# Kernel tuning notes

Hardware: AMD Instinct MI355X
Metric: run time of the kernel (lower is better)

## Reference

```python
import jax, jax.numpy as jnp
import numpy as np

N = 100000   # nodes
E = 1600000  # edges (avg degree 16)
D = 64       # input_dim
H = 64       # hidden_dim
C = 40       # num_classes
K = 2        # x_steps (KProp)


def setup_inputs() -> dict:
    key = jax.random.key(0)
    ks = jax.random.split(key, 8)
    x = jax.random.normal(ks[0], (N, D), dtype=jnp.float32)
    edge_src = jax.random.randint(ks[1], (E,), 0, N, dtype=jnp.int32)
    edge_dst = jax.random.randint(ks[2], (E,), 0, N, dtype=jnp.int32)
    def lin(k, fi, fo):
        b = 1.0 / np.sqrt(fi)
        return jax.random.uniform(k, (fi, fo), jnp.float32, -b, b)
    Wl1 = lin(ks[3], D, H)  # SAGEConv1 neighbor weight
    Wr1 = lin(ks[4], D, H)  # SAGEConv1 root weight
    b1 = jnp.zeros((H,), jnp.float32)
    Wl2 = lin(ks[5], H, C)
    Wr2 = lin(ks[6], H, C)
    b2 = jnp.zeros((C,), jnp.float32)
    return {"x": x, "Wl1": Wl1, "Wr1": Wr1, "b1": b1,
            "Wl2": Wl2, "Wr2": Wr2, "b2": b2,
            "edge_src": edge_src, "edge_dst": edge_dst}


def reference(x, Wl1, Wr1, b1, Wl2, Wr2, b2, edge_src, edge_dst):
    ones = jnp.ones((edge_src.shape[0],), x.dtype)
    deg = jax.ops.segment_sum(ones, edge_dst, num_segments=N)  # in-degree (adj_t row sums)
    # gcn_norm without self loops: w_e = deg[dst]^-1/2 * deg[src]^-1/2 (inf -> 0)
    dis = jnp.where(deg > 0, jax.lax.rsqrt(jnp.maximum(deg, 1.0)), 0.0)
    w = dis[edge_dst] * dis[edge_src]
    # KProp: K steps of normalized sparse matmul, 'add' aggregation
    h = x
    for _ in range(K):
        h = jax.ops.segment_sum(h[edge_src] * w[:, None], edge_dst, num_segments=N)
    cnt = jnp.maximum(deg, 1.0)[:, None]  # mean-aggr denominator (0-row safe)
    # SAGEConv1: lin_l(mean_neighbors) + lin_r(root), then selu (dropout p=0)
    agg1 = jax.ops.segment_sum(h[edge_src], edge_dst, num_segments=N) / cnt
    h1 = jax.nn.selu(agg1 @ Wl1 + h @ Wr1 + b1)
    # SAGEConv2
    agg2 = jax.ops.segment_sum(h1[edge_src], edge_dst, num_segments=N) / cnt
    out = agg2 @ Wl2 + h1 @ Wr2 + b2
    return jax.nn.softmax(out, axis=1)
```

## Files before the change

### kernel.cpp

```cpp
#include <hip/hip_runtime.h>
#include <hip/hip_bf16.h>
#include <math.h>


#define RFL(x) __builtin_amdgcn_readfirstlane(x)
#define BK_SHIFT 10
#define MAXBUCK 256

__device__ __forceinline__ float bf2f(unsigned short u) {
    return __uint_as_float((unsigned)u << 16);
}
__device__ __forceinline__ unsigned short f2bf(float f) {
    __hip_bfloat16 b = __float2bfloat16(f);
    return *reinterpret_cast<unsigned short*>(&b);
}


__global__ void init_bcursor_kernel(int* __restrict__ bcursor, int nbuck, int cap) {
    int i = blockIdx.x * blockDim.x + threadIdx.x;
    if (i < nbuck) bcursor[i] = i * cap;
}

__global__ __launch_bounds__(256) void partition_kernel(const int* __restrict__ src,
                                                        const int* __restrict__ dst,
                                                        int* __restrict__ bcursor,
                                                        unsigned int* __restrict__ temp,
                                                        int e, int nbuck, int cap) {
    __shared__ int bc[MAXBUCK];
    int t = threadIdx.x;
    int chunk = (e + gridDim.x - 1) / gridDim.x;
    int base = blockIdx.x * chunk;
    int cnt = e - base;
    if (cnt > chunk) cnt = chunk;
    if (cnt < 0) cnt = 0;
    for (int j = t; j < nbuck; j += 256) bc[j] = 0;
    __syncthreads();
    for (int i = t; i < cnt; i += 256) {
        int d = dst[base + i];
        atomicAdd(&bc[d >> BK_SHIFT], 1);
    }
    __syncthreads();
    for (int j = t; j < nbuck; j += 256) {
        int c = bc[j];
        bc[j] = (c > 0) ? atomicAdd(&bcursor[j], c) : 0;
    }
    __syncthreads();
    for (int i = t; i < cnt; i += 256) {
        int s = src[base + i];
        int d = dst[base + i];
        int bk = d >> BK_SHIFT;
        int p = atomicAdd(&bc[bk], 1);
        if (p < (bk + 1) * cap) temp[p] = ((unsigned int)s << BK_SHIFT) | (unsigned int)(d & 1023);
    }
}

__global__ __launch_bounds__(256) void bucket_csr_kernel(const unsigned int* __restrict__ temp,
                                                         const int* __restrict__ bcursor,
                                                         int* __restrict__ row_ptr,
                                                         float* __restrict__ dis,
                                                         float* __restrict__ cnt_inv,
                                                         int* __restrict__ csr_src,
                                                         int n, int cap, int nbuck, int e) {
    __shared__ int cnt3[1024];
    __shared__ int part[256];
    int b = blockIdx.x;
    int t = threadIdx.x;
    int nbeg = b << BK_SHIFT;
    int cj = 0;
    if (t < nbuck) {
        cj = bcursor[t] - t * cap;
        if (cj > cap) cj = cap;
    }
    part[t] = cj;
    __syncthreads();
    for (int off = 1; off < 256; off <<= 1) {
        int u = (t >= off) ? part[t - off] : 0;
        __syncthreads();
        part[t] += u;
        __syncthreads();
    }
    int cntb = bcursor[b] - b * cap;
    if (cntb > cap) cntb = cap;
    int bbase = part[b] - cntb;
    __syncthreads();
    for (int i = t; i < 1024; i += 256) cnt3[i] = 0;
    __syncthreads();
    const unsigned int* tb = temp + (size_t)b * cap;
    for (int i = t; i < cntb; i += 256) {
        atomicAdd(&cnt3[tb[i] & 1023u], 1);
    }
    __syncthreads();
    int d0 = cnt3[t * 4 + 0], d1 = cnt3[t * 4 + 1], d2 = cnt3[t * 4 + 2], d3 = cnt3[t * 4 + 3];
    int run = d0 + d1 + d2 + d3;
    int dd[4] = {d0, d1, d2, d3};
#pragma unroll
    for (int k = 0; k < 4; ++k) {
        int node = nbeg + t * 4 + k;
        if (node < n) {
            float fd = (float)dd[k];
            dis[node] = (dd[k] > 0) ? rsqrtf(fd) : 0.0f;
            cnt_inv[node] = 1.0f / fmaxf(fd, 1.0f);
        }
    }
    __syncthreads();
    part[t] = run;
    __syncthreads();
    for (int off = 1; off < 256; off <<= 1) {
        int u = (t >= off) ? part[t - off] : 0;
        __syncthreads();
        part[t] += u;
        __syncthreads();
    }
    int ex = part[t] - run;
    int oo[4];
    oo[0] = ex; oo[1] = ex + d0; oo[2] = ex + d0 + d1; oo[3] = ex + d0 + d1 + d2;
#pragma unroll
    for (int k = 0; k < 4; ++k) {
        cnt3[t * 4 + k] = oo[k];
        int node = nbeg + t * 4 + k;
        if (node < n) row_ptr[node] = bbase + oo[k];
    }
    if (b == nbuck - 1 && t == 0) row_ptr[n] = e;
    __syncthreads();
    for (int i = t; i < cntb; i += 256) {
        unsigned int ed = tb[i];
        int pos = atomicAdd(&cnt3[ed & 1023u], 1);
        csr_src[bbase + pos] = (int)(ed >> BK_SHIFT);
    }
}

__global__ void f2bf_kernel(const float4* __restrict__ in, ushort4* __restrict__ out, int n4) {
    int i = blockIdx.x * blockDim.x + threadIdx.x;
    if (i < n4) {
        float4 v = in[i];
        ushort4 u;
        u.x = f2bf(v.x); u.y = f2bf(v.y); u.z = f2bf(v.z); u.w = f2bf(v.w);
        out[i] = u;
    }
}

template <int TAG>
__global__ __launch_bounds__(256) void prop4bf_kernel(const ushort4* __restrict__ in4u,
                                                      ushort4* __restrict__ out4u,
                                                      const int* __restrict__ row_ptr,
                                                      const int* __restrict__ csr_src,
                                                      const float* __restrict__ dis,
                                                      int n) {
    int lane = threadIdx.x & 63;
    int g = lane >> 4;
    int l = lane & 15;
    int node = RFL(blockIdx.x * 4 + (threadIdx.x >> 6));
    if (node >= n) return;
    int beg = row_ptr[node];
    int end = row_ptr[node + 1];
    float4 acc = make_float4(0.f, 0.f, 0.f, 0.f);
    int j = beg;
    for (; j + 16 <= end; j += 16) {
        int s[4];
        ushort4 u[4];
        float w[4];
#pragma unroll
        for (int q = 0; q < 4; ++q) s[q] = csr_src[j + q * 4 + g];
#pragma unroll
        for (int q = 0; q < 4; ++q) u[q] = in4u[(size_t)s[q] * 16 + l];
#pragma unroll
        for (int q = 0; q < 4; ++q) w[q] = dis[s[q]];
#pragma unroll
        for (int q = 0; q < 4; ++q) {
            acc.x += w[q] * bf2f(u[q].x);
            acc.y += w[q] * bf2f(u[q].y);
            acc.z += w[q] * bf2f(u[q].z);
            acc.w += w[q] * bf2f(u[q].w);
        }
    }
    for (; j + 8 <= end; j += 8) {
        int s[2];
        ushort4 u[2];
        float w[2];
#pragma unroll
        for (int q = 0; q < 2; ++q) s[q] = csr_src[j + q * 4 + g];
#pragma unroll
        for (int q = 0; q < 2; ++q) u[q] = in4u[(size_t)s[q] * 16 + l];
#pragma unroll
        for (int q = 0; q < 2; ++q) w[q] = dis[s[q]];
#pragma unroll
        for (int q = 0; q < 2; ++q) {
            acc.x += w[q] * bf2f(u[q].x);
            acc.y += w[q] * bf2f(u[q].y);
            acc.z += w[q] * bf2f(u[q].z);
            acc.w += w[q] * bf2f(u[q].w);
        }
    }
    for (; j < end; j += 4) {
        int idx = j + g;
        bool valid = idx < end;
        int s = csr_src[valid ? idx : (end - 1)];
        float w = valid ? dis[s] : 0.0f;
        ushort4 u = in4u[(size_t)s * 16 + l];
        acc.x += w * bf2f(u.x);
        acc.y += w * bf2f(u.y);
        acc.z += w * bf2f(u.z);
        acc.w += w * bf2f(u.w);
    }
    acc.x += __shfl_xor(acc.x, 16); acc.x += __shfl_xor(acc.x, 32);
    acc.y += __shfl_xor(acc.y, 16); acc.y += __shfl_xor(acc.y, 32);
    acc.z += __shfl_xor(acc.z, 16); acc.z += __shfl_xor(acc.z, 32);
    acc.w += __shfl_xor(acc.w, 16); acc.w += __shfl_xor(acc.w, 32);
    if (g == 0) {
        float sc = dis[node];
        ushort4 o;
        o.x = f2bf(acc.x * sc);
        o.y = f2bf(acc.y * sc);
        o.z = f2bf(acc.z * sc);
        o.w = f2bf(acc.w * sc);
        out4u[(size_t)node * 16 + l] = o;
    }
}

__global__ __launch_bounds__(256) void prop_mean_bf_kernel(const ushort4* __restrict__ in4u,
                                                           ushort4* __restrict__ out4u,
                                                           const int* __restrict__ row_ptr,
                                                           const int* __restrict__ csr_src,
                                                           const float* __restrict__ cnt_inv,
                                                           const float4* __restrict__ r4,
                                                           const float4* __restrict__ b4,
                                                           int n) {
    int lane = threadIdx.x & 63;
    int g = lane >> 4;
    int l = lane & 15;
    int node = RFL(blockIdx.x * 4 + (threadIdx.x >> 6));
    if (node >= n) return;
    int beg = row_ptr[node];
    int end = row_ptr[node + 1];
    float4 acc = make_float4(0.f, 0.f, 0.f, 0.f);
    int j = beg;
    for (; j + 16 <= end; j += 16) {
        int s[4];
        ushort4 u[4];
#pragma unroll
        for (int q = 0; q < 4; ++q) s[q] = csr_src[j + q * 4 + g];
#pragma unroll
        for (int q = 0; q < 4; ++q) u[q] = in4u[(size_t)s[q] * 16 + l];
#pragma unroll
        for (int q = 0; q < 4; ++q) {
            acc.x += bf2f(u[q].x);
            acc.y += bf2f(u[q].y);
            acc.z += bf2f(u[q].z);
            acc.w += bf2f(u[q].w);
        }
    }
    for (; j + 8 <= end; j += 8) {
        int s[2];
        ushort4 u[2];
#pragma unroll
        for (int q = 0; q < 2; ++q) s[q] = csr_src[j + q * 4 + g];
#pragma unroll
        for (int q = 0; q < 2; ++q) u[q] = in4u[(size_t)s[q] * 16 + l];
#pragma unroll
        for (int q = 0; q < 2; ++q) {
            acc.x += bf2f(u[q].x);
            acc.y += bf2f(u[q].y);
            acc.z += bf2f(u[q].z);
            acc.w += bf2f(u[q].w);
        }
    }
    for (; j < end; j += 4) {
        int idx = j + g;
        bool valid = idx < end;
        int s = csr_src[valid ? idx : (end - 1)];
        float w = valid ? 1.0f : 0.0f;
        ushort4 u = in4u[(size_t)s * 16 + l];
        acc.x += w * bf2f(u.x);
        acc.y += w * bf2f(u.y);
        acc.z += w * bf2f(u.z);
        acc.w += w * bf2f(u.w);
    }
    acc.x += __shfl_xor(acc.x, 16); acc.x += __shfl_xor(acc.x, 32);
    acc.y += __shfl_xor(acc.y, 16); acc.y += __shfl_xor(acc.y, 32);
    acc.z += __shfl_xor(acc.z, 16); acc.z += __shfl_xor(acc.z, 32);
    acc.w += __shfl_xor(acc.w, 16); acc.w += __shfl_xor(acc.w, 32);
    if (g == 0) {
        float sc = cnt_inv[node];
        float4 ra = r4[(size_t)node * 16 + l];
        float4 bb = b4[l];
        const float scale = 1.0507009873554805f;
        const float alpha = 1.6732632423543772f;
        float t0 = acc.x * sc + ra.x + bb.x;
        float t1 = acc.y * sc + ra.y + bb.y;
        float t2 = acc.z * sc + ra.z + bb.z;
        float t3 = acc.w * sc + ra.w + bb.w;
        t0 = scale * (t0 > 0.0f ? t0 : alpha * expm1f(t0));
        t1 = scale * (t1 > 0.0f ? t1 : alpha * expm1f(t1));
        t2 = scale * (t2 > 0.0f ? t2 : alpha * expm1f(t2));
        t3 = scale * (t3 > 0.0f ? t3 : alpha * expm1f(t3));
        ushort4 o;
        o.x = f2bf(t0); o.y = f2bf(t1); o.z = f2bf(t2); o.w = f2bf(t3);
        out4u[(size_t)node * 16 + l] = o;
    }
}

__global__ __launch_bounds__(256) void prop_softmax_bf_kernel(const ushort4* __restrict__ in4u,
                                                              float* __restrict__ out,
                                                              const int* __restrict__ row_ptr,
                                                              const int* __restrict__ csr_src,
                                                              const float* __restrict__ cnt_inv,
                                                              const float* __restrict__ r_add,
                                                              int n) {
    int lane = threadIdx.x & 63;
    int g = lane >> 4;
    int l = lane & 15;
    bool act = l < 10;
    int node = RFL(blockIdx.x * 4 + (threadIdx.x >> 6));
    if (node >= n) return;
    int beg = row_ptr[node];
    int end = row_ptr[node + 1];
    float4 acc = make_float4(0.f, 0.f, 0.f, 0.f);
    const ushort4 uz = make_ushort4(0, 0, 0, 0);
    int j = beg;
    for (; j + 16 <= end; j += 16) {
        int s[4];
        ushort4 u[4] = {uz, uz, uz, uz};
#pragma unroll
        for (int q = 0; q < 4; ++q) s[q] = csr_src[j + q * 4 + g];
        if (act) {
#pragma unroll
            for (int q = 0; q < 4; ++q) u[q] = in4u[(size_t)s[q] * 10 + l];
        }
#pragma unroll
        for (int q = 0; q < 4; ++q) {
            acc.x += bf2f(u[q].x);
            acc.y += bf2f(u[q].y);
            acc.z += bf2f(u[q].z);
            acc.w += bf2f(u[q].w);
        }
    }
    for (; j + 8 <= end; j += 8) {
        int s[2];
        ushort4 u[2] = {uz, uz};
#pragma unroll
        for (int q = 0; q < 2; ++q) s[q] = csr_src[j + q * 4 + g];
        if (act) {
#pragma unroll
            for (int q = 0; q < 2; ++q) u[q] = in4u[(size_t)s[q] * 10 + l];
        }
#pragma unroll
        for (int q = 0; q < 2; ++q) {
            acc.x += bf2f(u[q].x);
            acc.y += bf2f(u[q].y);
            acc.z += bf2f(u[q].z);
            acc.w += bf2f(u[q].w);
        }
    }
    for (; j < end; j += 4) {
        int idx = j + g;
        bool valid = idx < end;
        int s = csr_src[valid ? idx : (end - 1)];
        if (act) {
            ushort4 u = in4u[(size_t)s * 10 + l];
            float w = valid ? 1.0f : 0.0f;
            acc.x += w * bf2f(u.x);
            acc.y += w * bf2f(u.y);
            acc.z += w * bf2f(u.z);
            acc.w += w * bf2f(u.w);
        }
    }
    acc.x += __shfl_xor(acc.x, 16); acc.x += __shfl_xor(acc.x, 32);
    acc.y += __shfl_xor(acc.y, 16); acc.y += __shfl_xor(acc.y, 32);
    acc.z += __shfl_xor(acc.z, 16); acc.z += __shfl_xor(acc.z, 32);
    acc.w += __shfl_xor(acc.w, 16); acc.w += __shfl_xor(acc.w, 32);
    if (g == 0) {
        float sc = cnt_inv[node];
        float4 ra = act ? reinterpret_cast<const float4*>(r_add)[(size_t)node * 10 + l]
                        : make_float4(0.f, 0.f, 0.f, 0.f);
        float t0 = acc.x * sc + ra.x;
        float t1 = acc.y * sc + ra.y;
        float t2 = acc.z * sc + ra.z;
        float t3 = acc.w * sc + ra.w;
        float m = act ? fmaxf(fmaxf(t0, t1), fmaxf(t2, t3)) : -INFINITY;
        m = fmaxf(m, __shfl_xor(m, 1));
        m = fmaxf(m, __shfl_xor(m, 2));
        m = fmaxf(m, __shfl_xor(m, 4));
        m = fmaxf(m, __shfl_xor(m, 8));
        float e0 = act ? __expf(t0 - m) : 0.0f;
        float e1 = act ? __expf(t1 - m) : 0.0f;
        float e2 = act ? __expf(t2 - m) : 0.0f;
        float e3 = act ? __expf(t3 - m) : 0.0f;
        float s = e0 + e1 + e2 + e3;
        s += __shfl_xor(s, 1);
        s += __shfl_xor(s, 2);
        s += __shfl_xor(s, 4);
        s += __shfl_xor(s, 8);
        if (act) {
            float inv = 1.0f / s;
            float4 o;
            o.x = e0 * inv; o.y = e1 * inv; o.z = e2 * inv; o.w = e3 * inv;
            reinterpret_cast<float4*>(out)[(size_t)node * 10 + l] = o;
        }
    }
}

template <int OC, int CP>
__global__ __launch_bounds__(256) void gemm_kernel(const unsigned short* __restrict__ in,
                                                   const float* __restrict__ Wl,
                                                   const float* __restrict__ Wr,
                                                   const float* __restrict__ bias,
                                                   __hip_bfloat16* __restrict__ outL,
                                                   float* __restrict__ outR,
                                                   int n, int add_bias) {
    constexpr int HC = OC / 2;
    constexpr int TX = OC / CP;
    constexpr int TY = 256 / TX;
    constexpr int NPT = 64 / TY;
    constexpr int XP = 68;
    constexpr int WP = OC + 4;
    __shared__ float sXT[64 * XP];
    __shared__ float sW[64 * WP];
    int t = threadIdx.x;
    int blk = blockIdx.x;
    for (int i = 0; i < 16; ++i) {
        int idx = i * 256 + t;
        int nd = idx >> 6;
        int k = idx & 63;
        int ng = blk * 64 + nd;
        float v = bf2f(in[(size_t)(ng < n ? ng : n - 1) * 64 + k]);
        sXT[k * XP + nd] = v;
    }
    for (int i = t; i < 64 * HC; i += 256) {
        int k = i / HC;
        int c = i % HC;
        sW[k * WP + c] = Wl[i];
        sW[k * WP + HC + c] = Wr[i];
    }
    __syncthreads();
    int tx = t % TX;
    int ty = t / TX;
    float acc[NPT][CP];
#pragma unroll
    for (int i = 0; i < NPT; ++i)
#pragma unroll
        for (int c = 0; c < CP; ++c) acc[i][c] = 0.0f;
#pragma unroll 4
    for (int k = 0; k < 64; ++k) {
        float xv[NPT];
#pragma unroll
        for (int i = 0; i < NPT; ++i) xv[i] = sXT[k * XP + ty * NPT + i];
        float wv[CP];
#pragma unroll
        for (int c = 0; c < CP; ++c) wv[c] = sW[k * WP + tx + TX * c];
#pragma unroll
        for (int i = 0; i < NPT; ++i)
#pragma unroll
            for (int c = 0; c < CP; ++c) acc[i][c] += xv[i] * wv[c];
    }
#pragma unroll
    for (int i = 0; i < NPT; ++i) {
        int ng = blk * 64 + ty * NPT + i;
        if (ng >= n) break;
#pragma unroll
        for (int c = 0; c < CP; ++c) {
            int col = tx + TX * c;
            if (col < HC) {
                outL[(size_t)ng * HC + col] = __float2bfloat16(acc[i][c]);
            } else {
                float v = acc[i][c] + (add_bias ? bias[col - HC] : 0.0f);
                outR[(size_t)ng * HC + (col - HC)] = v;
            }
        }
    }
}


extern "C" void kernel_launch(void* const* d_in, const int* in_sizes, int n_in,
                              void* d_out, int out_size, void* d_ws, size_t ws_size,
                              hipStream_t stream) {
    const float* x   = (const float*)d_in[0];
    const float* Wl1 = (const float*)d_in[1];
    const float* Wr1 = (const float*)d_in[2];
    const float* b1  = (const float*)d_in[3];
    const float* Wl2 = (const float*)d_in[4];
    const float* Wr2 = (const float*)d_in[5];
    const float* b2  = (const float*)d_in[6];
    const int* edge_src = (const int*)d_in[7];
    const int* edge_dst = (const int*)d_in[8];
    float* out = (float*)d_out;

    const int N = in_sizes[0] / 64;
    const int E = in_sizes[7];
    const int NBUCK = (N + (1 << BK_SHIFT) - 1) >> BK_SHIFT;
    size_t buf_bytes = (size_t)N * 64 * 4;
    int cap = E / NBUCK + E / (2 * NBUCK) + 1024;
    int cap_max = (int)(buf_bytes / ((size_t)NBUCK * 4));
    if (cap > cap_max) cap = cap_max;

    size_t off = 0;
    auto carve = [&](size_t bytes) -> void* {
        void* p = (char*)d_ws + off;
        off = (off + bytes + 255) & ~(size_t)255;
        return p;
    };
    int*          row_ptr = (int*)carve((size_t)(N + 1) * 4);
    int*          bcursor = (int*)carve((size_t)NBUCK * 4);
    float*        dis     = (float*)carve((size_t)N * 4);
    float*        cnt_inv = (float*)carve((size_t)N * 4);
    int*          csr_src = (int*)carve((size_t)E * 4);
    char*         bufA    = (char*)carve(buf_bytes);
    char*         bufB    = (char*)carve(buf_bytes);
    float*        bufC    = (float*)carve(buf_bytes);
    unsigned int* temp    = (unsigned int*)bufC;
    (void)ws_size;

    unsigned short* xb  = (unsigned short*)bufA;
    unsigned short* p0b = (unsigned short*)(bufA + buf_bytes / 2);
    unsigned short* hb  = (unsigned short*)bufB;
    unsigned short* t1b = (unsigned short*)bufA;
    unsigned short* h1b = (unsigned short*)bufB;
    unsigned short* t2b = (unsigned short*)(bufA + buf_bytes / 2);

    const int nb_node = (N + 3) / 4;
    const int nb_gemm = (N + 63) / 64;
    const int n4 = N * 64 / 4;

    init_bcursor_kernel<<<(NBUCK + 255) / 256, 256, 0, stream>>>(bcursor, NBUCK, cap);
    partition_kernel<<<256, 256, 0, stream>>>(edge_src, edge_dst, bcursor, temp, E, NBUCK, cap);
    bucket_csr_kernel<<<NBUCK, 256, 0, stream>>>(temp, bcursor, row_ptr, dis, cnt_inv,
                                                 csr_src, N, cap, NBUCK, E);

    f2bf_kernel<<<(n4 + 255) / 256, 256, 0, stream>>>((const float4*)x, (ushort4*)xb, n4);
    prop4bf_kernel<1><<<nb_node, 256, 0, stream>>>((const ushort4*)xb, (ushort4*)p0b,
                                                   row_ptr, csr_src, dis, N);
    prop4bf_kernel<2><<<nb_node, 256, 0, stream>>>((const ushort4*)p0b, (ushort4*)hb,
                                                   row_ptr, csr_src, dis, N);
    gemm_kernel<128, 8><<<nb_gemm, 256, 0, stream>>>(hb, Wl1, Wr1, nullptr,
                                                     (__hip_bfloat16*)t1b, bufC, N, 0);
    prop_mean_bf_kernel<<<nb_node, 256, 0, stream>>>((const ushort4*)t1b, (ushort4*)h1b,
                                                     row_ptr, csr_src, cnt_inv,
                                                     (const float4*)bufC, (const float4*)b1, N);
    gemm_kernel<80, 5><<<nb_gemm, 256, 0, stream>>>(h1b, Wl2, Wr2, b2,
                                                    (__hip_bfloat16*)t2b, bufC, N, 1);
    prop_softmax_bf_kernel<<<nb_node, 256, 0, stream>>>((const ushort4*)t2b, out, row_ptr,
                                                        csr_src, cnt_inv, bufC, N);
}
```

Before: 392.9 us.

## Replace scalar FP32 dense GEMMs with bf16 MFMA kernels using split weights

Replaces the two shared-memory FP32 FMA GEMM kernels with a matrix-core version built on mfma_f32_16x16x32_bf16. Inputs are loaded into LDS with an XOR swizzle, and weights are split into bf16 high and residual parts to keep near-FP32 weight precision. The goal is to cut compute and LDS traffic in the GEMM stages. These GEMMs are only a small part of a pipeline dominated by sparse gathers, so the overall effect is likely small, and the extra weight conversion per block adds overhead.

```diff
diff --git a/kernel.cpp b/kernel.cpp
--- a/kernel.cpp
+++ b/kernel.cpp
@@ -6,6 +6,10 @@
 #define RFL(x) __builtin_amdgcn_readfirstlane(x)
 #define BK_SHIFT 10
 #define MAXBUCK 256
+
+typedef short bf16x8 __attribute__((ext_vector_type(8)));
+typedef float f32x4 __attribute__((ext_vector_type(4)));
+typedef unsigned short ushort8v __attribute__((ext_vector_type(8)));
 
 __device__ __forceinline__ float bf2f(unsigned short u) {
     return __uint_as_float((unsigned)u << 16);
@@ -399,71 +403,82 @@
     }
 }
 
-template <int OC, int CP>
-__global__ __launch_bounds__(256) void gemm_kernel(const unsigned short* __restrict__ in,
-                                                   const float* __restrict__ Wl,
-                                                   const float* __restrict__ Wr,
-                                                   const float* __restrict__ bias,
-                                                   __hip_bfloat16* __restrict__ outL,
-                                                   float* __restrict__ outR,
-                                                   int n, int add_bias) {
+template <int OC>
+__global__ __launch_bounds__(256) void gemm_mfma_kernel(const unsigned short* __restrict__ in,
+                                                        const float* __restrict__ Wl,
+                                                        const float* __restrict__ Wr,
+                                                        const float* __restrict__ bias,
+                                                        __hip_bfloat16* __restrict__ outL,
+                                                        float* __restrict__ outR,
+                                                        int n, int add_bias) {
     constexpr int HC = OC / 2;
-    constexpr int TX = OC / CP;
-    constexpr int TY = 256 / TX;
-    constexpr int NPT = 64 / TY;
-    constexpr int XP = 68;
-    constexpr int WP = OC + 4;
-    __shared__ float sXT[64 * XP];
-    __shared__ float sW[64 * WP];
+    constexpr int NF = OC / 16;
+    __shared__ unsigned short sA[64 * 64];
+    __shared__ unsigned short sBh[OC * 64];
+    __shared__ unsigned short sBr[OC * 64];
     int t = threadIdx.x;
     int blk = blockIdx.x;
-    for (int i = 0; i < 16; ++i) {
+
+#pragma unroll
+    for (int i = 0; i < 2; ++i) {
         int idx = i * 256 + t;
-        int nd = idx >> 6;
-        int k = idx & 63;
-        int ng = blk * 64 + nd;
-        float v = bf2f(in[(size_t)(ng < n ? ng : n - 1) * 64 + k]);
-        sXT[k * XP + nd] = v;
-    }
-    for (int i = t; i < 64 * HC; i += 256) {
-        int k = i / HC;
-        int c = i % HC;
-        sW[k * WP + c] = Wl[i];
-        sW[k * WP + HC + c] = Wr[i];
-    }
-    __syncthreads();
-    int tx = t % TX;
-    int ty = t / TX;
-    float acc[NPT][CP];
-#pragma unroll
-    for (int i = 0; i < NPT; ++i)
-#pragma unroll
-        for (int c = 0; c < CP; ++c) acc[i][c] = 0.0f;
-#pragma unroll 4
-    for (int k = 0; k < 64; ++k) {
-        float xv[NPT];
-#pragma unroll
-        for (int i = 0; i < NPT; ++i) xv[i] = sXT[k * XP + ty * NPT + i];
-        float wv[CP];
-#pragma unroll
-        for (int c = 0; c < CP; ++c) wv[c] = sW[k * WP + tx + TX * c];
-#pragma unroll
-        for (int i = 0; i < NPT; ++i)
-#pragma unroll
-            for (int c = 0; c < CP; ++c) acc[i][c] += xv[i] * wv[c];
-    }
-#pragma unroll
-    for (int i = 0; i < NPT; ++i) {
-        int ng = blk * 64 + ty * NPT + i;
-        if (ng >= n) break;
-#pragma unroll
-        for (int c = 0; c < CP; ++c) {
-            int col = tx + TX * c;
-            if (col < HC) {
-                outL[(size_t)ng * HC + col] = __float2bfloat16(acc[i][c]);
-            } else {
-                float v = acc[i][c] + (add_bias ? bias[col - HC] : 0.0f);
-                outR[(size_t)ng * HC + (col - HC)] = v;
+        int m = idx >> 3;
+        int kb = idx & 7;
+        int node = blk * 64 + m;
+        if (node >= n) node = n - 1;
+        ushort8v v = *reinterpret_cast<const ushort8v*>(in + (size_t)node * 64 + kb * 8);
+        *reinterpret_cast<ushort8v*>(&sA[m * 64 + ((kb ^ (m & 7)) << 3)]) = v;
+    }
+    for (int idx = t; idx < 64 * OC; idx += 256) {
+        int k = idx / OC;
+        int c = idx - k * OC;
+        float v = (c < HC) ? Wl[k * HC + c] : Wr[k * HC + (c - HC)];
+        unsigned short hi = f2bf(v);
+        unsigned short re = f2bf(v - bf2f(hi));
+        int pos = c * 64 + (((k >> 3) ^ (c & 7)) << 3) + (k & 7);
+        sBh[pos] = hi;
+        sBr[pos] = re;
+    }
+    __syncthreads();
+
+    int w = t >> 6;
+    int lane = t & 63;
+    int r = lane & 15;
+    int q = lane >> 4;
+    int m = w * 16 + r;
+    bf16x8 A0 = *reinterpret_cast<const bf16x8*>(&sA[m * 64 + (((0 + q) ^ (r & 7)) << 3)]);
+    bf16x8 A1 = *reinterpret_cast<const bf16x8*>(&sA[m * 64 + (((4 + q) ^ (r & 7)) << 3)]);
+
+    f32x4 acc[NF];
+#pragma unroll
+    for (int c = 0; c < NF; ++c) acc[c] = (f32x4)(0.0f);
+
+#pragma unroll
+    for (int c = 0; c < NF; ++c) {
+        int cb = c * 16 + r;
+        bf16x8 B0 = *reinterpret_cast<const bf16x8*>(&sBh[cb * 64 + (((0 + q) ^ (r & 7)) << 3)]);
+        bf16x8 B1 = *reinterpret_cast<const bf16x8*>(&sBh[cb * 64 + (((4 + q) ^ (r & 7)) << 3)]);
+        bf16x8 R0 = *reinterpret_cast<const bf16x8*>(&sBr[cb * 64 + (((0 + q) ^ (r & 7)) << 3)]);
+        bf16x8 R1 = *reinterpret_cast<const bf16x8*>(&sBr[cb * 64 + (((4 + q) ^ (r & 7)) << 3)]);
+        acc[c] = __builtin_amdgcn_mfma_f32_16x16x32_bf16(A0, B0, acc[c], 0, 0, 0);
+        acc[c] = __builtin_amdgcn_mfma_f32_16x16x32_bf16(A1, B1, acc[c], 0, 0, 0);
+        acc[c] = __builtin_amdgcn_mfma_f32_16x16x32_bf16(A0, R0, acc[c], 0, 0, 0);
+        acc[c] = __builtin_amdgcn_mfma_f32_16x16x32_bf16(A1, R1, acc[c], 0, 0, 0);
+    }
+
+#pragma unroll
+    for (int c = 0; c < NF; ++c) {
+        int col = c * 16 + r;
+#pragma unroll
+        for (int j = 0; j < 4; ++j) {
+            int node = blk * 64 + w * 16 + q * 4 + j;
+            if (node < n) {
+                float v = acc[c][j];
+                if (col < HC) {
+                    outL[(size_t)node * HC + col] = __float2bfloat16(v);
+                } else {
+                    outR[(size_t)node * HC + (col - HC)] = v + (add_bias ? bias[col - HC] : 0.0f);
+                }
             }
         }
     }
@@ -530,13 +545,13 @@
                                                    row_ptr, csr_src, dis, N);
     prop4bf_kernel<2><<<nb_node, 256, 0, stream>>>((const ushort4*)p0b, (ushort4*)hb,
                                                    row_ptr, csr_src, dis, N);
-    gemm_kernel<128, 8><<<nb_gemm, 256, 0, stream>>>(hb, Wl1, Wr1, nullptr,
-                                                     (__hip_bfloat16*)t1b, bufC, N, 0);
+    gemm_mfma_kernel<128><<<nb_gemm, 256, 0, stream>>>(hb, Wl1, Wr1, nullptr,
+                                                       (__hip_bfloat16*)t1b, bufC, N, 0);
     prop_mean_bf_kernel<<<nb_node, 256, 0, stream>>>((const ushort4*)t1b, (ushort4*)h1b,
                                                      row_ptr, csr_src, cnt_inv,
                                                      (const float4*)bufC, (const float4*)b1, N);
-    gemm_kernel<80, 5><<<nb_gemm, 256, 0, stream>>>(h1b, Wl2, Wr2, b2,
-                                                    (__hip_bfloat16*)t2b, bufC, N, 1);
+    gemm_mfma_kernel<80><<<nb_gemm, 256, 0, stream>>>(h1b, Wl2, Wr2, b2,
+                                                      (__hip_bfloat16*)t2b, bufC, N, 1);
     prop_softmax_bf_kernel<<<nb_node, 256, 0, stream>>>((const ushort4*)t2b, out, row_ptr,
                                                         csr_src, cnt_inv, bufC, N);
 }
```

New measurement: 368.1 us. -6.3%, faster.
